# Kernel tuning notes

Hardware: AMD Instinct MI355X
Metric: run time of the kernel (lower is better)

The kernel has to match this reference:

```python
import jax, jax.numpy as jnp
import numpy as np

NUM_USERS = 50000
NUM_ITEMS = 20000
N_NODES = NUM_USERS + NUM_ITEMS
D = 128
CONTENT_DIM = 512
BATCH = 8192
N_EDGES = 500000
NEG_SLOPE = 0.2  # GATConv leaky_relu slope


def setup_inputs() -> dict:
    key = jax.random.key(0)
    ks = jax.random.split(key, 16)
    return {
        "user_ids": jax.random.randint(ks[0], (BATCH,), 0, NUM_USERS),
        "item_ids": jax.random.randint(ks[1], (BATCH,), 0, NUM_ITEMS),
        "content_features": jax.random.normal(ks[2], (BATCH, CONTENT_DIM), jnp.float32),
        "edge_index": jax.random.randint(ks[3], (2, N_EDGES), 0, N_NODES),
        "user_emb_w": jax.random.normal(ks[4], (NUM_USERS, D), jnp.float32) * 0.05,
        "item_emb_w": jax.random.normal(ks[5], (NUM_ITEMS, D), jnp.float32) * 0.05,
        "content_proj_w": jax.random.normal(ks[6], (D, CONTENT_DIM), jnp.float32) * 0.04,
        "content_proj_b": jnp.zeros((D,), jnp.float32),
        "conv1_lin_w": jax.random.normal(ks[7], (2 * D, 2 * D), jnp.float32) * 0.06,
        "conv1_att_src": jax.random.normal(ks[8], (2, D), jnp.float32) * 0.1,
        "conv1_att_dst": jax.random.normal(ks[9], (2, D), jnp.float32) * 0.1,
        "conv1_bias": jnp.zeros((2 * D,), jnp.float32),
        "conv2_lin_w": jax.random.normal(ks[10], (D, 2 * D), jnp.float32) * 0.06,
        "conv2_att_src": jax.random.normal(ks[11], (1, D), jnp.float32) * 0.1,
        "conv2_att_dst": jax.random.normal(ks[12], (1, D), jnp.float32) * 0.1,
        "conv2_bias": jnp.zeros((D,), jnp.float32),
        "pred_w1": jax.random.normal(ks[13], (D, 3 * D), jnp.float32) * 0.05,
        "pred_b1": jnp.zeros((D,), jnp.float32),
        "pred_w2": jax.random.normal(ks[14], (1, D), jnp.float32) * 0.09,
        "pred_b2": jnp.zeros((1,), jnp.float32),
    }


def gat_conv(x, src, dst, lin_w, att_src, att_dst, bias, heads, out_ch):
    # PyG GATConv (shared lin for src/dst, concat=True, add_self_loops handled outside)
    n = x.shape[0]
    h = (x @ lin_w.T).reshape(n, heads, out_ch)          # [N,H,C]
    a_src = jnp.sum(h * att_src, axis=-1)                # [N,H]
    a_dst = jnp.sum(h * att_dst, axis=-1)                # [N,H]
    alpha = jax.nn.leaky_relu(a_src[src] + a_dst[dst], NEG_SLOPE)  # [E,H]
    # softmax over incoming edges of each destination node
    amax = jax.ops.segment_max(alpha, dst, num_segments=n)
    ex = jnp.exp(alpha - amax[dst])
    denom = jax.ops.segment_sum(ex, dst, num_segments=n)
    w = ex / denom[dst]                                  # [E,H]
    out = jax.ops.segment_sum(h[src] * w[:, :, None], dst, num_segments=n)
    return out.reshape(n, heads * out_ch) + bias


def _forward(user_ids, item_ids, edge_index, content_features, user_emb_w, item_emb_w,
             content_proj_w, content_proj_b, conv1_lin_w, conv1_att_src, conv1_att_dst,
             conv1_bias, conv2_lin_w, conv2_att_src, conv2_att_dst, conv2_bias,
             pred_w1, pred_b1, pred_w2, pred_b2):
    u_emb = user_emb_w[user_ids]                         # [B,D]
    i_emb = item_emb_w[item_ids]                         # [B,D]
    c_emb = content_features @ content_proj_w.T + content_proj_b  # [B,D]
    # scatter-init sparse node features (only batch nodes are nonzero, as in source)
    x = jnp.zeros((N_NODES, 2 * D), jnp.float32)
    x = x.at[user_ids].set(jnp.concatenate([u_emb, jnp.zeros_like(c_emb)], axis=1))
    x = x.at[NUM_USERS + item_ids].set(jnp.concatenate([i_emb, c_emb], axis=1))
    # add self loops (fill_value irrelevant: edge_weight unused by GATConv)
    loops = jnp.arange(N_NODES, dtype=edge_index.dtype)
    src = jnp.concatenate([edge_index[0], loops])
    dst = jnp.concatenate([edge_index[1], loops])
    x = jax.nn.elu(gat_conv(x, src, dst, conv1_lin_w, conv1_att_src, conv1_att_dst, conv1_bias, 2, D))
    # dropout inactive (eval mode)
    x = gat_conv(x, src, dst, conv2_lin_w, conv2_att_src, conv2_att_dst, conv2_bias, 1, D)
    combined = jnp.concatenate([u_emb, x[NUM_USERS + item_ids], x[user_ids]], axis=1)  # [B,3D]
    h = jax.nn.relu(combined @ pred_w1.T + pred_b1)
    return (h @ pred_w2.T + pred_b2).squeeze(-1)         # [B]


def reference(user_ids, item_ids, content_features, edge_index, user_emb_w, item_emb_w,
              content_proj_w, content_proj_b, conv1_lin_w, conv1_att_src, conv1_att_dst,
              conv1_bias, conv2_lin_w, conv2_att_src, conv2_att_dst, conv2_bias,
              pred_w1, pred_b1, pred_w2, pred_b2):
    return _forward(user_ids, item_ids, edge_index, content_features, user_emb_w, item_emb_w,
                    content_proj_w, content_proj_b, conv1_lin_w, conv1_att_src, conv1_att_dst,
                    conv1_bias, conv2_lin_w, conv2_att_src, conv2_att_dst, conv2_bias,
                    pred_w1, pred_b1, pred_w2, pred_b2)
```

## Files before the change

### kernel.cpp

```cpp
#include <hip/hip_runtime.h>
#include <hip/hip_bf16.h>

#define NU 50000
#define NI 20000
#define NN 70000
#define DD 128
#define BB 8192
#define EE 500000
#define ET 570000
#define NTASK 16384

__device__ __forceinline__ float lrelu(float x) { return x > 0.f ? x : 0.2f * x; }

typedef __attribute__((ext_vector_type(8))) short bf16x8;
typedef __attribute__((ext_vector_type(8))) unsigned short u16x8;
typedef __attribute__((ext_vector_type(4))) float f32x4;

__device__ __forceinline__ unsigned short f2bf_rne(float f) {
  unsigned int u = __builtin_bit_cast(unsigned int, f);
  u += 0x7FFFu + ((u >> 16) & 1u);
  return (unsigned short)(u >> 16);
}
__device__ __forceinline__ float bf2f(unsigned short h) {
  unsigned int u = ((unsigned int)h) << 16;
  return __builtin_bit_cast(float, u);
}

template <int GATHER, int MODE>
__global__ __launch_bounds__(256) void gemm_mfma(
    const float* __restrict__ A,
    const unsigned short* __restrict__ Bh, const unsigned short* __restrict__ Bl,
    const float* __restrict__ bias, float* __restrict__ C,
    unsigned short* __restrict__ Cb, int ldc,
    int M, int N, int K, int act,
    const int* __restrict__ idx0, const int* __restrict__ idx1,
    const int* __restrict__ mapv,
    const float* __restrict__ gA0, const float* __restrict__ gA1,
    const float* __restrict__ att_s, const float* __restrict__ att_d,
    float* __restrict__ a1s, float* __restrict__ a1d) {
  __shared__ __align__(16) unsigned short sAh[8][64][8];
  __shared__ __align__(16) unsigned short sAl[8][64][8];
  __shared__ __align__(16) unsigned short sBh[8][64][8];
  __shared__ __align__(16) unsigned short sBl[8][64][8];
  int tid = threadIdx.x;
  int bm = blockIdx.x * 64, bn = blockIdx.y * 64;
  int lane = tid & 63, w = tid >> 6;
  int wr = (w >> 1) * 32, wc = (w & 1) * 32;
  int fr = lane & 15, fk = lane >> 4;
  f32x4 acc[2][2] = {};

  for (int k0 = 0; k0 < K; k0 += 64) {
    __syncthreads();
#pragma unroll
    for (int t = 0; t < 2; t++) {
      int f = tid + t * 256;
      int row = f >> 3, kb = f & 7;
      int kg = k0 + kb * 8;
      const float* ap;
      if (GATHER == 1) {
        int sec = kg >> 7;
        int kc = kg & 127;
        int r = bm + row;
        if (sec == 0)      ap = &gA0[(size_t)idx0[r] * 128 + kc];
        else if (sec == 1) ap = &gA1[(size_t)mapv[NU + idx1[r]] * 128 + kc];
        else               ap = &gA1[(size_t)mapv[idx0[r]] * 128 + kc];
      } else if (GATHER == 2) {
        ap = &gA0[(size_t)idx0[bm + row] * K + kg];
      } else {
        ap = &A[(size_t)(bm + row) * K + kg];
      }
      float4 v0 = *reinterpret_cast<const float4*>(ap);
      float4 v1 = *reinterpret_cast<const float4*>(ap + 4);
      float vv[8] = {v0.x, v0.y, v0.z, v0.w, v1.x, v1.y, v1.z, v1.w};
      u16x8 hv, lv;
#pragma unroll
      for (int j = 0; j < 8; j++) {
        unsigned short hh = f2bf_rne(vv[j]);
        hv[j] = hh;
        lv[j] = (unsigned short)(__builtin_bit_cast(unsigned int, vv[j] - bf2f(hh)) >> 16);
      }
      *reinterpret_cast<u16x8*>(&sAh[kb][row][0]) = hv;
      *reinterpret_cast<u16x8*>(&sAl[kb][row][0]) = lv;
    }
#pragma unroll
    for (int t = 0; t < 2; t++) {
      int f = tid + t * 256;
      int row = f >> 3, kb = f & 7;
      int kg = k0 + kb * 8;
      *reinterpret_cast<u16x8*>(&sBh[kb][row][0]) =
          *reinterpret_cast<const u16x8*>(&Bh[(size_t)(bn + row) * K + kg]);
      *reinterpret_cast<u16x8*>(&sBl[kb][row][0]) =
          *reinterpret_cast<const u16x8*>(&Bl[(size_t)(bn + row) * K + kg]);
    }
    __syncthreads();
#pragma unroll
    for (int s = 0; s < 2; s++) {
      int kb = s * 4 + fk;
      bf16x8 ah0 = *reinterpret_cast<const bf16x8*>(&sAh[kb][wr + fr][0]);
// ... 29 lines not shown
      for (int i = 0; i < 2; i++) {
#pragma unroll
        for (int r = 0; r < 4; r++) {
          float v = acc[i][j][r];
          ps[i][r] += v * asc;
          pd[i][r] += v * adc;
          Cb[(size_t)(bm + wr + i * 16 + fk * 4 + r) * ldc + col] = f2bf_rne(v);
        }
      }
    }
#pragma unroll
    for (int o = 1; o < 16; o <<= 1) {
#pragma unroll
      for (int i = 0; i < 2; i++)
#pragma unroll
        for (int r = 0; r < 4; r++) {
          ps[i][r] += __shfl_xor(ps[i][r], o);
          pd[i][r] += __shfl_xor(pd[i][r], o);
        }
    }
    if (fr == 0) {
#pragma unroll
      for (int i = 0; i < 2; i++) {
#pragma unroll
        for (int r = 0; r < 4; r++) {
          int t = bm + wr + i * 16 + fk * 4 + r;
          int v = (t < BB) ? idx0[t] : NU + idx1[t - BB];
          if (mapv[v] == t) {
            atomicAdd(&a1s[(size_t)v * 2 + head], ps[i][r]);
            atomicAdd(&a1d[(size_t)v * 2 + head], pd[i][r]);
          }
        }
      }
    }
    return;
  }
#pragma unroll
  for (int j = 0; j < 2; j++) {
    int col = bn + wc + j * 16 + fr;
    float bj = bias ? bias[col] : 0.f;
#pragma unroll
    for (int i = 0; i < 2; i++) {
#pragma unroll
      for (int r = 0; r < 4; r++) {
        int row = bm + wr + i * 16 + fk * 4 + r;
        float v = acc[i][j][r] + bj;
        if (act == 1) v = fmaxf(v, 0.f);
        C[(size_t)row * ldc + col] = v;
      }
    }
  }
}

#define EB 2227
#define SPLB 832
#define XAB 4096
__global__ __launch_bounds__(256) void setup_kernel(
    const int* __restrict__ ei, const int* __restrict__ uid, const int* __restrict__ iid,
    int* __restrict__ deg, int* __restrict__ winner,
    const float* __restrict__ wc, unsigned short* wch, unsigned short* wcl,
    const float* __restrict__ w1, unsigned short* w1h, unsigned short* w1l,
    const float* __restrict__ w2, unsigned short* w2h, unsigned short* w2l,
    const float* __restrict__ pw1, unsigned short* p1h, unsigned short* p1l,
    const float* __restrict__ uemb, const float* __restrict__ iemb,
    float* __restrict__ Xa, int* __restrict__ map) {
  int bid = blockIdx.x, tid = threadIdx.x;
  if (bid < EB) {
    int e = bid * 256 + tid;
    if (e < BB) atomicMax(&winner[iid[e]], e);
    if (e >= ET) return;
    int dst = (e < EE) ? ei[EE + e] : (e - EE);
    atomicAdd(&deg[dst], 1);
    return;
  }
  if (bid < EB + SPLB) {
    int i = (bid - EB) * 256 + tid;
    const float* w; unsigned short* h; unsigned short* l; int idx;
    if (i < 65536) { w = wc; h = wch; l = wcl; idx = i; }
    else if (i < 131072) { w = w1; h = w1h; l = w1l; idx = i - 65536; }
    else if (i < 163840) { w = w2; h = w2h; l = w2l; idx = i - 131072; }
    else { w = pw1; h = p1h; l = p1l; idx = i - 163840; }
    float f = w[idx];
    unsigned short hh = f2bf_rne(f);
    h[idx] = hh;
    l[idx] = (unsigned short)(__builtin_bit_cast(unsigned int, f - bf2f(hh)) >> 16);
    return;
  }
  int t = (bid - EB - SPLB) * 4 + (tid >> 6);
  int lane = tid & 63;
  int c4 = lane * 4;
  if (t < BB) {
    int u = uid[t];
    float4 v = make_float4(0.f, 0.f, 0.f, 0.f);
    if (c4 < DD) v = *reinterpret_cast<const float4*>(&uemb[(size_t)u * DD + c4]);
    *reinterpret_cast<float4*>(&Xa[(size_t)t * 256 + c4]) = v;
    if (lane == 0) map[u] = t;
  } else {
    int it = iid[t - BB];
    if (c4 < DD) {
      float4 v = *reinterpret_cast<const float4*>(&iemb[(size_t)it * DD + c4]);
      *reinterpret_cast<float4*>(&Xa[(size_t)t * 256 + c4]) = v;
    }
    if (lane == 0) map[NU + it] = t;
  }
}

__global__ void rowstart_kernel(const int* __restrict__ deg, const int* __restrict__ winner,
                                const int* __restrict__ iid,
                                int* __restrict__ rowstart, int* __restrict__ fill,
                                int* __restrict__ counter, int* __restrict__ widx,
                                const float* __restrict__ w2,
                                const float* __restrict__ att2s, const float* __restrict__ att2d,
                                float* __restrict__ qs, float* __restrict__ qd) {
  int blk = blockIdx.x;
  if (blk == (NN + 255) / 256) {
    int k = threadIdx.x;
    float s = 0.f, d = 0.f;
#pragma unroll 4
    for (int j = 0; j < DD; j++) {
      float w = w2[(size_t)j * 256 + k];
      s += att2s[j] * w;
      d += att2d[j] * w;
    }
    qs[k] = s;
    qd[k] = d;
    return;
  }
  int v = blk * 256 + threadIdx.x;
  if (v < BB) widx[v] = winner[iid[v]];
  if (v >= NN) return;
  int s = atomicAdd(counter, deg[v]);
  rowstart[v] = s;
  fill[v] = s;
}

__global__ void fill_mark_kernel(const int* __restrict__ ei, int* __restrict__ fill,
                                 int* __restrict__ col, const int* __restrict__ map,
                                 unsigned char* __restrict__ needed) {
  int e = blockIdx.x * 256 + threadIdx.x;
  if (e >= ET) return;
  int src, dst;
  if (e < EE) { src = ei[e]; dst = ei[EE + e]; }
  else { src = e - EE; dst = src; }
  int pos = atomicAdd(&fill[dst], 1);
  col[pos] = src;
  if (map[dst] >= 0) needed[src] = 1;
}

__global__ __launch_bounds__(256) void conv1_agg_kernel(
    const int* __restrict__ col, const int* __restrict__ rowstart,
    const int* __restrict__ deg, const unsigned short* __restrict__ Hb,
    const int* __restrict__ map, const unsigned char* __restrict__ needed,
    const float* __restrict__ a1s, const float* __restrict__ a1d,
    const float* __restrict__ bias,
    const float* __restrict__ qs, const float* __restrict__ qd,
    unsigned short* __restrict__ x1b, float* __restrict__ a2s, float* __restrict__ a2d) {
  int v = blockIdx.x * 4 + (threadIdx.x >> 6);
  int lane = threadIdx.x & 63;
  if (!needed[v]) return;
  int head = lane >> 5;
  int d = deg[v], s0 = rowstart[v];
  float2 adv = *reinterpret_cast<const float2*>(&a1d[(size_t)v * 2]);
  float4 acc = make_float4(0.f, 0.f, 0.f, 0.f);
  float den;
  if (d <= 64) {
    bool act = lane < d;
    int ci = act ? col[s0 + lane] : 0;
    float2 asv = make_float2(0.f, 0.f);
    int ri = -1;
    if (act) {
      asv = *reinterpret_cast<const float2*>(&a1s[(size_t)ci * 2]);
      ri = map[ci];
    }
    float al0 = act ? lrelu(asv.x + adv.x) : -1e30f;
    float al1 = act ? lrelu(asv.y + adv.y) : -1e30f;
    float m0 = al0, m1 = al1;
#pragma unroll
    for (int o = 1; o < 64; o <<= 1) {
      m0 = fmaxf(m0, __shfl_xor(m0, o));
      m1 = fmaxf(m1, __shfl_xor(m1, o));
    }
    float ex0 = act ? __expf(al0 - m0) : 0.f;
    float ex1 = act ? __expf(al1 - m1) : 0.f;
    float cs0 = ex0, cs1 = ex1;
#pragma unroll
    for (int o = 1; o < 64; o <<= 1) {
      cs0 += __shfl_xor(cs0, o);
      cs1 += __shfl_xor(cs1, o);
    }
    den = head ? cs1 : cs0;
    for (int i2 = 0; i2 < d; i2++) {
      int r = __shfl(ri, i2);
      if (r >= 0) {
        float e0 = __shfl(ex0, i2), e1 = __shfl(ex1, i2);
        float ex = head ? e1 : e0;
        ushort4 hv = *reinterpret_cast<const ushort4*>(&Hb[((size_t)r << 8) + (lane << 2)]);
        acc.x += ex * bf2f(hv.x); acc.y += ex * bf2f(hv.y);
        acc.z += ex * bf2f(hv.z); acc.w += ex * bf2f(hv.w);
      }
    }
  } else {
    float m0 = -1e30f, m1 = -1e30f, den0 = 0.f, den1 = 0.f;
    for (int c0 = 0; c0 < d; c0 += 64) {
      int i = c0 + lane;
      bool act = i < d;
      int ci = act ? col[s0 + i] : 0;
      float2 asv = make_float2(0.f, 0.f);
      int ri = -1;
      if (act) {
        asv = *reinterpret_cast<const float2*>(&a1s[(size_t)ci * 2]);
        ri = map[ci];
      }
      float al0 = act ? lrelu(asv.x + adv.x) : -1e30f;
      float al1 = act ? lrelu(asv.y + adv.y) : -1e30f;
      float cm0 = al0, cm1 = al1;
#pragma unroll
      for (int o = 1; o < 64; o <<= 1) {
        cm0 = fmaxf(cm0, __shfl_xor(cm0, o));
        cm1 = fmaxf(cm1, __shfl_xor(cm1, o));
      }
      float nm0 = fmaxf(m0, cm0), nm1 = fmaxf(m1, cm1);
      float ex0 = act ? __expf(al0 - nm0) : 0.f;
      float ex1 = act ? __expf(al1 - nm1) : 0.f;
      float s0f = __expf(m0 - nm0), s1f = __expf(m1 - nm1);
      float cs0 = ex0, cs1 = ex1;
#pragma unroll
      for (int o = 1; o < 64; o <<= 1) {
        cs0 += __shfl_xor(cs0, o);
        cs1 += __shfl_xor(cs1, o);
      }
      den0 = den0 * s0f + cs0;
      den1 = den1 * s1f + cs1;
      float sc = head ? s1f : s0f;
      acc.x *= sc; acc.y *= sc; acc.z *= sc; acc.w *= sc;
      int n = min(64, d - c0);
      for (int i2 = 0; i2 < n; i2++) {
        int r = __shfl(ri, i2);
        if (r >= 0) {
          float e0 = __shfl(ex0, i2), e1 = __shfl(ex1, i2);
          float ex = head ? e1 : e0;
          ushort4 hv = *reinterpret_cast<const ushort4*>(&Hb[((size_t)r << 8) + (lane << 2)]);
          acc.x += ex * bf2f(hv.x); acc.y += ex * bf2f(hv.y);
          acc.z += ex * bf2f(hv.z); acc.w += ex * bf2f(hv.w);
        }
      }
      m0 = nm0; m1 = nm1;
    }
    den = head ? den1 : den0;
  }
  float inv = 1.f / den;
  float4 b4 = *reinterpret_cast<const float4*>(&bias[lane << 2]);
  float4 o;
  o.x = fmaf(acc.x, inv, b4.x);
  o.y = fmaf(acc.y, inv, b4.y);
  o.z = fmaf(acc.z, inv, b4.z);
  o.w = fmaf(acc.w, inv, b4.w);
  o.x = o.x > 0.f ? o.x : __expf(o.x) - 1.f;
  o.y = o.y > 0.f ? o.y : __expf(o.y) - 1.f;
  o.z = o.z > 0.f ? o.z : __expf(o.z) - 1.f;
  o.w = o.w > 0.f ? o.w : __expf(o.w) - 1.f;
  ushort4 st;
  st.x = f2bf_rne(o.x); st.y = f2bf_rne(o.y);
  st.z = f2bf_rne(o.z); st.w = f2bf_rne(o.w);
  *reinterpret_cast<ushort4*>(&x1b[((size_t)v << 8) + (lane << 2)]) = st;
  float4 sv = *reinterpret_cast<const float4*>(&qs[lane << 2]);
  float4 dv = *reinterpret_cast<const float4*>(&qd[lane << 2]);
  float ps = o.x * sv.x + o.y * sv.y + o.z * sv.z + o.w * sv.w;
  float pd = o.x * dv.x + o.y * dv.y + o.z * dv.z + o.w * dv.w;
#pragma unroll
  for (int of = 1; of < 64; of <<= 1) { ps += __shfl_xor(ps, of); pd += __shfl_xor(pd, of); }
  if (lane == 0) { a2s[v] = ps; a2d[v] = pd; }
}

__global__ __launch_bounds__(256) void conv2_agg_kernel(
    const int* __restrict__ uid, const int* __restrict__ iid,
    const int* __restrict__ col, const int* __restrict__ rowstart,
    const int* __restrict__ deg, const int* __restrict__ map,
    const unsigned short* __restrict__ x1b,
    const float* __restrict__ a2s, const float* __restrict__ a2d,
    float* __restrict__ agg) {
  int t = blockIdx.x * 4 + (threadIdx.x >> 6);
  int lane = threadIdx.x & 63;
  int v = (t < BB) ? uid[t] : NU + iid[t - BB];
  if (map[v] != t) return;
  int d = deg[v], s0 = rowstart[v];
  float ad = a2d[v];
  float4 acc = make_float4(0.f, 0.f, 0.f, 0.f);
  float den;
  if (d <= 64) {
    bool act = lane < d;
    int ci = act ? col[s0 + lane] : 0;
    float as = act ? a2s[ci] : 0.f;
    float al = act ? lrelu(as + ad) : -1e30f;
    float m = al;
#pragma unroll
    for (int o = 1; o < 64; o <<= 1) m = fmaxf(m, __shfl_xor(m, o));
    float ex = act ? __expf(al - m) : 0.f;
    float cs = ex;
#pragma unroll
    for (int o = 1; o < 64; o <<= 1) cs += __shfl_xor(cs, o);
    den = cs;
    for (int i2 = 0; i2 < d; i2++) {
      int r = __shfl(ci, i2);
      float e = __shfl(ex, i2);
      ushort4 hv = *reinterpret_cast<const ushort4*>(&x1b[((size_t)r << 8) + (lane << 2)]);
      acc.x += e * bf2f(hv.x); acc.y += e * bf2f(hv.y);
      acc.z += e * bf2f(hv.z); acc.w += e * bf2f(hv.w);
    }
  } else {
    float m = -1e30f; den = 0.f;
    for (int c0 = 0; c0 < d; c0 += 64) {
      int i = c0 + lane;
      bool act = i < d;
      int ci = act ? col[s0 + i] : 0;
      float as = act ? a2s[ci] : 0.f;
      float al = act ? lrelu(as + ad) : -1e30f;
      float cm = al;
#pragma unroll
      for (int o = 1; o < 64; o <<= 1) cm = fmaxf(cm, __shfl_xor(cm, o));
      float nm = fmaxf(m, cm);
      float ex = act ? __expf(al - nm) : 0.f;
      float sf = __expf(m - nm);
      float cs = ex;
#pragma unroll
      for (int o = 1; o < 64; o <<= 1) cs += __shfl_xor(cs, o);
      den = den * sf + cs;
      acc.x *= sf; acc.y *= sf; acc.z *= sf; acc.w *= sf;
      int n = min(64, d - c0);
      for (int i2 = 0; i2 < n; i2++) {
        int r = __shfl(ci, i2);
        float e = __shfl(ex, i2);
        ushort4 hv = *reinterpret_cast<const ushort4*>(&x1b[((size_t)r << 8) + (lane << 2)]);
        acc.x += e * bf2f(hv.x); acc.y += e * bf2f(hv.y);
        acc.z += e * bf2f(hv.z); acc.w += e * bf2f(hv.w);
      }
      m = nm;
    }
  }
  float inv = 1.f / den;
  float4 o = make_float4(acc.x * inv, acc.y * inv, acc.z * inv, acc.w * inv);
  *reinterpret_cast<float4*>(&agg[((size_t)t << 8) + (lane << 2)]) = o;
}

__global__ __launch_bounds__(256) void final_kernel(
    const float* __restrict__ ph, const float* __restrict__ w2,
    const float* __restrict__ b2, float* __restrict__ out) {
  int b = blockIdx.x * 4 + (threadIdx.x >> 6);
  int lane = threadIdx.x & 63;
  float2 hv = *reinterpret_cast<const float2*>(&ph[((size_t)b << 7) + (lane << 1)]);
  float2 wv = *reinterpret_cast<const float2*>(&w2[lane << 1]);
  float s = hv.x * wv.x + hv.y * wv.y;
  for (int o = 1; o < 64; o <<= 1) s += __shfl_xor(s, o);
  if (lane == 0) out[b] = s + b2[0];
}

extern "C" void kernel_launch(void* const* d_in, const int* in_sizes, int n_in,
                              void* d_out, int out_size, void* d_ws, size_t ws_size,
                              hipStream_t stream) {
  const int* uid = (const int*)d_in[0];
  const int* iid = (const int*)d_in[1];
  const float* content = (const float*)d_in[2];
  const int* ei = (const int*)d_in[3];
  const float* uemb = (const float*)d_in[4];
  const float* iemb = (const float*)d_in[5];
  const float* wc = (const float*)d_in[6];
  const float* bc = (const float*)d_in[7];
  const float* w1 = (const float*)d_in[8];
  const float* att1s = (const float*)d_in[9];
  const float* att1d = (const float*)d_in[10];
  const float* b1 = (const float*)d_in[11];
  const float* w2 = (const float*)d_in[12];
  const float* att2s = (const float*)d_in[13];
  const float* att2d = (const float*)d_in[14];
  const float* b2c = (const float*)d_in[15];
  const float* pw1 = (const float*)d_in[16];
  const float* pb1 = (const float*)d_in[17];
  const float* pw2 = (const float*)d_in[18];
  const float* pb2 = (const float*)d_in[19];
  float* out = (float*)d_out;
  char* ws = (char*)d_ws;

  size_t off = 0;
  auto alloc = [&](size_t bytes) {
    size_t o = off;
    off += (bytes + 255) & ~(size_t)255;
    return o;
  };
  size_t o_winner  = alloc(NI * 4);
  size_t o_map     = alloc(NN * 4);
  size_t o_a1s     = alloc((size_t)NN * 2 * 4);
  size_t o_a1d     = alloc((size_t)NN * 2 * 4);
  size_t o_deg     = alloc(NN * 4);
  size_t o_rs      = alloc(NN * 4);
  size_t o_fill    = alloc(NN * 4);
  size_t o_cnt     = alloc(4);
  size_t o_needed  = alloc(NN);
  size_t o_col     = alloc((size_t)ET * 4);
  size_t o_a2s     = alloc(NN * 4);
  size_t o_a2d     = alloc(NN * 4);
  size_t o_qs      = alloc(256 * 4);
  size_t o_qd      = alloc(256 * 4);
  size_t o_widx    = alloc(BB * 4);
  size_t o_wch = alloc(65536 * 2),  o_wcl = alloc(65536 * 2);
  size_t o_w1h = alloc(65536 * 2),  o_w1l = alloc(65536 * 2);
  size_t o_w2h = alloc(32768 * 2),  o_w2l = alloc(32768 * 2);
  size_t o_p1h = alloc(49152 * 2),  o_p1l = alloc(49152 * 2);
  size_t o_r1    = alloc(16777216 + 8388608);
  size_t o_xa    = o_r1;
  size_t o_hb    = o_r1 + 16777216;
  size_t o_agg   = o_r1;
  size_t o_out2c = o_r1 + 16777216;
  size_t o_ph    = o_r1;
  size_t o_x1b   = alloc((size_t)NN * 256 * 2);
  (void)ws_size; (void)in_sizes; (void)n_in; (void)out_size;

  int*   winner = (int*)(ws + o_winner);
  int*   map    = (int*)(ws + o_map);
  float* a1s    = (float*)(ws + o_a1s);
  float* a1d    = (float*)(ws + o_a1d);
  int*   deg    = (int*)(ws + o_deg);
  int*   rs     = (int*)(ws + o_rs);
  int*   fill   = (int*)(ws + o_fill);
  int*   cnt    = (int*)(ws + o_cnt);
  unsigned char* needed = (unsigned char*)(ws + o_needed);
  int*   col    = (int*)(ws + o_col);
  float* a2s    = (float*)(ws + o_a2s);
  float* a2d    = (float*)(ws + o_a2d);
  float* qs     = (float*)(ws + o_qs);
  float* qd     = (float*)(ws + o_qd);
  int*   widx   = (int*)(ws + o_widx);
  unsigned short* wch = (unsigned short*)(ws + o_wch);
  unsigned short* wcl = (unsigned short*)(ws + o_wcl);
  unsigned short* w1h = (unsigned short*)(ws + o_w1h);
  unsigned short* w1l = (unsigned short*)(ws + o_w1l);
  unsigned short* w2h = (unsigned short*)(ws + o_w2h);
  unsigned short* w2l = (unsigned short*)(ws + o_w2l);
  unsigned short* p1h = (unsigned short*)(ws + o_p1h);
  unsigned short* p1l = (unsigned short*)(ws + o_p1l);
  float* Xa     = (float*)(ws + o_xa);
  unsigned short* Hb = (unsigned short*)(ws + o_hb);
  float* agg    = (float*)(ws + o_agg);
  float* out2c  = (float*)(ws + o_out2c);
  float* ph     = (float*)(ws + o_ph);
  unsigned short* x1b = (unsigned short*)(ws + o_x1b);

  hipMemsetAsync(ws + o_winner, 0xFF, o_map - o_winner + (size_t)NN * 4, stream);
  hipMemsetAsync(ws + o_a1s, 0, o_a1d - o_a1s + (size_t)NN * 2 * 4, stream);
  hipMemsetAsync(ws + o_deg, 0, o_needed - o_deg + NN, stream);

  setup_kernel<<<EB + SPLB + XAB, 256, 0, stream>>>(
      ei, uid, iid, deg, winner,
      wc, wch, wcl, w1, w1h, w1l, w2, w2h, w2l, pw1, p1h, p1l,
      uemb, iemb, Xa, map);
  rowstart_kernel<<<(NN + 255) / 256 + 1, 256, 0, stream>>>(
      deg, winner, iid, rs, fill, cnt, widx, w2, att2s, att2d, qs, qd);
  {
    dim3 g(BB / 64, DD / 64);
    gemm_mfma<2, 0><<<g, 256, 0, stream>>>(
        nullptr, wch, wcl, bc, Xa + (size_t)BB * 256 + 128, nullptr, 256,
        BB, DD, 512, 0, widx, nullptr, nullptr, content, nullptr,
        nullptr, nullptr, nullptr, nullptr);
  }
  fill_mark_kernel<<<(ET + 255) / 256, 256, 0, stream>>>(ei, fill, col, map, needed);
  {
    dim3 g(NTASK / 64, 256 / 64);
    gemm_mfma<0, 1><<<g, 256, 0, stream>>>(
        Xa, w1h, w1l, nullptr, nullptr, Hb, 256,
        NTASK, 256, 256, 0, uid, iid, map, nullptr, nullptr,
        att1s, att1d, a1s, a1d);
  }
  conv1_agg_kernel<<<NN / 4, 256, 0, stream>>>(col, rs, deg, Hb, map, needed,
                                               a1s, a1d, b1, qs, qd, x1b, a2s, a2d);
  conv2_agg_kernel<<<NTASK / 4, 256, 0, stream>>>(uid, iid, col, rs, deg, map,
                                                  x1b, a2s, a2d, agg);
  {
    dim3 g(NTASK / 64, DD / 64);
    gemm_mfma<0, 0><<<g, 256, 0, stream>>>(
        agg, w2h, w2l, b2c, out2c, nullptr, 128,
        NTASK, DD, 256, 0, nullptr, nullptr, nullptr, nullptr, nullptr,
        nullptr, nullptr, nullptr, nullptr);
  }
  {
    dim3 g(BB / 64, DD / 64);
    gemm_mfma<1, 0><<<g, 256, 0, stream>>>(
        nullptr, p1h, p1l, pb1, ph, nullptr, 128,
        BB, DD, 384, 1, uid, iid, map, uemb, out2c,
        nullptr, nullptr, nullptr, nullptr);
  }
  final_kernel<<<BB / 4, 256, 0, stream>>>(ph, pw2, pb2, out);
}
```

Baseline: 220.5 us.

## Merge content GEMM with CSR fill and widen gather loads in aggregation

The content-projection GEMM and the CSR fill/mark pass are now one launch: the first blocks run the GEMM tile and the rest do the edge scatter, so the two independent stages can overlap and one launch is saved. In both GAT aggregation kernels, each half-wave now handles alternate neighbours with 16-byte bf16 loads (8 features per lane), and the two halves are combined with a cross-half shuffle at the end. This halves the serial neighbour loop length and widens the loads, at the cost of more registers and an extra reduction step.

```diff
diff --git a/kernel.cpp b/kernel.cpp
--- a/kernel.cpp
+++ b/kernel.cpp
@@ -27,7 +27,8 @@
 }
 
 template <int GATHER, int MODE>
-__global__ __launch_bounds__(256) void gemm_mfma(
+__device__ __forceinline__ void gemm_core(
+    int bm, int bn,
     const float* __restrict__ A,
     const unsigned short* __restrict__ Bh, const unsigned short* __restrict__ Bl,
     const float* __restrict__ bias, float* __restrict__ C,
@@ -43,7 +44,6 @@
   __shared__ __align__(16) unsigned short sBh[8][64][8];
   __shared__ __align__(16) unsigned short sBl[8][64][8];
   int tid = threadIdx.x;
-  int bm = blockIdx.x * 64, bn = blockIdx.y * 64;
   int lane = tid & 63, w = tid >> 6;
   int wr = (w >> 1) * 32, wc = (w & 1) * 32;
   int fr = lane & 15, fk = lane >> 4;
@@ -179,6 +179,48 @@
   }
 }
 
+template <int GATHER, int MODE>
+__global__ __launch_bounds__(256) void gemm_mfma(
+    const float* __restrict__ A,
+    const unsigned short* __restrict__ Bh, const unsigned short* __restrict__ Bl,
+    const float* __restrict__ bias, float* __restrict__ C,
+    unsigned short* __restrict__ Cb, int ldc,
+    int M, int N, int K, int act,
+    const int* __restrict__ idx0, const int* __restrict__ idx1,
+    const int* __restrict__ mapv,
+    const float* __restrict__ gA0, const float* __restrict__ gA1,
+    const float* __restrict__ att_s, const float* __restrict__ att_d,
+    float* __restrict__ a1s, float* __restrict__ a1d) {
+  gemm_core<GATHER, MODE>(blockIdx.x * 64, blockIdx.y * 64,
+                          A, Bh, Bl, bias, C, Cb, ldc, M, N, K, act,
+                          idx0, idx1, mapv, gA0, gA1, att_s, att_d, a1s, a1d);
+}
+
+#define GEMMB 256
+__global__ __launch_bounds__(256) void cembfill_kernel(
+    const unsigned short* __restrict__ wch, const unsigned short* __restrict__ wcl,
+    const float* __restrict__ bc, float* __restrict__ XaC,
+    const int* __restrict__ widx, const float* __restrict__ content,
+    const int* __restrict__ ei, int* __restrict__ fill, int* __restrict__ col,
+    const int* __restrict__ mapv, unsigned char* __restrict__ needed) {
+  int bid = blockIdx.x;
+  if (bid < GEMMB) {
+    gemm_core<2, 0>((bid >> 1) * 64, (bid & 1) * 64,
+                    nullptr, wch, wcl, bc, XaC, nullptr, 256,
+                    BB, DD, 512, 0, widx, nullptr, nullptr, content, nullptr,
+                    nullptr, nullptr, nullptr, nullptr);
+    return;
+  }
+  int e = (bid - GEMMB) * 256 + threadIdx.x;
+  if (e >= ET) return;
+  int src, dst;
+  if (e < EE) { src = ei[e]; dst = ei[EE + e]; }
+  else { src = e - EE; dst = src; }
+  int pos = atomicAdd(&fill[dst], 1);
+  col[pos] = src;
+  if (mapv[dst] >= 0) needed[src] = 1;
+}
+
 #define EB 2227
 #define SPLB 832
 #define XAB 4096
@@ -261,19 +303,6 @@
   fill[v] = s;
 }
 
-__global__ void fill_mark_kernel(const int* __restrict__ ei, int* __restrict__ fill,
-                                 int* __restrict__ col, const int* __restrict__ map,
-                                 unsigned char* __restrict__ needed) {
-  int e = blockIdx.x * 256 + threadIdx.x;
-  if (e >= ET) return;
-  int src, dst;
-  if (e < EE) { src = ei[e]; dst = ei[EE + e]; }
-  else { src = e - EE; dst = src; }
-  int pos = atomicAdd(&fill[dst], 1);
-  col[pos] = src;
-  if (map[dst] >= 0) needed[src] = 1;
-}
-
 __global__ __launch_bounds__(256) void conv1_agg_kernel(
     const int* __restrict__ col, const int* __restrict__ rowstart,
     const int* __restrict__ deg, const unsigned short* __restrict__ Hb,
@@ -285,10 +314,12 @@
   int v = blockIdx.x * 4 + (threadIdx.x >> 6);
   int lane = threadIdx.x & 63;
   if (!needed[v]) return;
-  int head = lane >> 5;
+  int half = lane >> 5;
+  int sub = lane & 31;
+  int chead = sub >> 4;
   int d = deg[v], s0 = rowstart[v];
   float2 adv = *reinterpret_cast<const float2*>(&a1d[(size_t)v * 2]);
-  float4 acc = make_float4(0.f, 0.f, 0.f, 0.f);
+  float acc[8] = {};
   float den;
   if (d <= 64) {
     bool act = lane < d;
@@ -315,15 +346,17 @@
       cs0 += __shfl_xor(cs0, o);
       cs1 += __shfl_xor(cs1, o);
     }
-    den = head ? cs1 : cs0;
-    for (int i2 = 0; i2 < d; i2++) {
-      int r = __shfl(ri, i2);
+    den = chead ? cs1 : cs0;
+    int nIt = (d + 1) >> 1;
+    for (int i2 = 0; i2 < nIt; i2++) {
+      int s = 2 * i2 + half;
+      int r = __shfl(ri, s);
+      float e0 = __shfl(ex0, s), e1 = __shfl(ex1, s);
+      float ex = chead ? e1 : e0;
       if (r >= 0) {
-        float e0 = __shfl(ex0, i2), e1 = __shfl(ex1, i2);
-        float ex = head ? e1 : e0;
-        ushort4 hv = *reinterpret_cast<const ushort4*>(&Hb[((size_t)r << 8) + (lane << 2)]);
-        acc.x += ex * bf2f(hv.x); acc.y += ex * bf2f(hv.y);
-        acc.z += ex * bf2f(hv.z); acc.w += ex * bf2f(hv.w);
+        u16x8 hv = *reinterpret_cast<const u16x8*>(&Hb[((size_t)r << 8) + (sub << 3)]);
+#pragma unroll
+        for (int k = 0; k < 8; k++) acc[k] += ex * bf2f(hv[k]);
       }
     }
   } else {
@@ -358,44 +391,50 @@
       }
       den0 = den0 * s0f + cs0;
       den1 = den1 * s1f + cs1;
-      float sc = head ? s1f : s0f;
-      acc.x *= sc; acc.y *= sc; acc.z *= sc; acc.w *= sc;
+      float sc = chead ? s1f : s0f;
+#pragma unroll
+      for (int k = 0; k < 8; k++) acc[k] *= sc;
       int n = min(64, d - c0);
-      for (int i2 = 0; i2 < n; i2++) {
-        int r = __shfl(ri, i2);
+      int nIt = (n + 1) >> 1;
+      for (int i2 = 0; i2 < nIt; i2++) {
+        int s = 2 * i2 + half;
+        int r = __shfl(ri, s);
+        float e0 = __shfl(ex0, s), e1 = __shfl(ex1, s);
+        float ex = chead ? e1 : e0;
         if (r >= 0) {
-          float e0 = __shfl(ex0, i2), e1 = __shfl(ex1, i2);
-          float ex = head ? e1 : e0;
-          ushort4 hv = *reinterpret_cast<const ushort4*>(&Hb[((size_t)r << 8) + (lane << 2)]);
-          acc.x += ex * bf2f(hv.x); acc.y += ex * bf2f(hv.y);
-          acc.z += ex * bf2f(hv.z); acc.w += ex * bf2f(hv.w);
+          u16x8 hv = *reinterpret_cast<const u16x8*>(&Hb[((size_t)r << 8) + (sub << 3)]);
+#pragma unroll
+          for (int k = 0; k < 8; k++) acc[k] += ex * bf2f(hv[k]);
         }
       }
       m0 = nm0; m1 = nm1;
     }
-    den = head ? den1 : den0;
-  }
+    den = chead ? den1 : den0;
+  }
+#pragma unroll
+  for (int k = 0; k < 8; k++) acc[k] += __shfl_xor(acc[k], 32);
   float inv = 1.f / den;
-  float4 b4 = *reinterpret_cast<const float4*>(&bias[lane << 2]);
-  float4 o;
-  o.x = fmaf(acc.x, inv, b4.x);
-  o.y = fmaf(acc.y, inv, b4.y);
-  o.z = fmaf(acc.z, inv, b4.z);
-  o.w = fmaf(acc.w, inv, b4.w);
-  o.x = o.x > 0.f ? o.x : __expf(o.x) - 1.f;
-  o.y = o.y > 0.f ? o.y : __expf(o.y) - 1.f;
-  o.z = o.z > 0.f ? o.z : __expf(o.z) - 1.f;
-  o.w = o.w > 0.f ? o.w : __expf(o.w) - 1.f;
+  float o[8];
+  float4 b4a = *reinterpret_cast<const float4*>(&bias[sub << 3]);
+  float4 b4b = *reinterpret_cast<const float4*>(&bias[(sub << 3) + 4]);
+  float bb[8] = {b4a.x, b4a.y, b4a.z, b4a.w, b4b.x, b4b.y, b4b.z, b4b.w};
+#pragma unroll
+  for (int k = 0; k < 8; k++) {
+    float t = fmaf(acc[k], inv, bb[k]);
+    o[k] = t > 0.f ? t : __expf(t) - 1.f;
+  }
   ushort4 st;
-  st.x = f2bf_rne(o.x); st.y = f2bf_rne(o.y);
-  st.z = f2bf_rne(o.z); st.w = f2bf_rne(o.w);
-  *reinterpret_cast<ushort4*>(&x1b[((size_t)v << 8) + (lane << 2)]) = st;
-  float4 sv = *reinterpret_cast<const float4*>(&qs[lane << 2]);
-  float4 dv = *reinterpret_cast<const float4*>(&qd[lane << 2]);
-  float ps = o.x * sv.x + o.y * sv.y + o.z * sv.z + o.w * sv.w;
-  float pd = o.x * dv.x + o.y * dv.y + o.z * dv.z + o.w * dv.w;
-#pragma unroll
-  for (int of = 1; of < 64; of <<= 1) { ps += __shfl_xor(ps, of); pd += __shfl_xor(pd, of); }
+  st.x = f2bf_rne(o[half * 4 + 0]); st.y = f2bf_rne(o[half * 4 + 1]);
+  st.z = f2bf_rne(o[half * 4 + 2]); st.w = f2bf_rne(o[half * 4 + 3]);
+  *reinterpret_cast<ushort4*>(&x1b[((size_t)v << 8) + (sub << 3) + half * 4]) = st;
+  float ps = 0.f, pd = 0.f;
+#pragma unroll
+  for (int k = 0; k < 8; k++) {
+    ps += o[k] * qs[(sub << 3) + k];
+    pd += o[k] * qd[(sub << 3) + k];
+  }
+#pragma unroll
+  for (int of = 1; of < 32; of <<= 1) { ps += __shfl_xor(ps, of); pd += __shfl_xor(pd, of); }
   if (lane == 0) { a2s[v] = ps; a2d[v] = pd; }
 }
 
@@ -410,9 +449,10 @@
   int lane = threadIdx.x & 63;
   int v = (t < BB) ? uid[t] : NU + iid[t - BB];
   if (map[v] != t) return;
+  int half = lane >> 5, sub = lane & 31;
   int d = deg[v], s0 = rowstart[v];
   float ad = a2d[v];
-  float4 acc = make_float4(0.f, 0.f, 0.f, 0.f);
+  float acc[8] = {};
   float den;
   if (d <= 64) {
     bool act = lane < d;
@@ -427,12 +467,14 @@
 #pragma unroll
     for (int o = 1; o < 64; o <<= 1) cs += __shfl_xor(cs, o);
     den = cs;
-    for (int i2 = 0; i2 < d; i2++) {
-      int r = __shfl(ci, i2);
-      float e = __shfl(ex, i2);
-      ushort4 hv = *reinterpret_cast<const ushort4*>(&x1b[((size_t)r << 8) + (lane << 2)]);
-      acc.x += e * bf2f(hv.x); acc.y += e * bf2f(hv.y);
-      acc.z += e * bf2f(hv.z); acc.w += e * bf2f(hv.w);
+    int nIt = (d + 1) >> 1;
+    for (int i2 = 0; i2 < nIt; i2++) {
+      int s = 2 * i2 + half;
+      int r = __shfl(ci, s);
+      float e = __shfl(ex, s);
+      u16x8 hv = *reinterpret_cast<const u16x8*>(&x1b[((size_t)r << 8) + (sub << 3)]);
+#pragma unroll
+      for (int k = 0; k < 8; k++) acc[k] += e * bf2f(hv[k]);
     }
   } else {
     float m = -1e30f; den = 0.f;
@@ -452,21 +494,28 @@
 #pragma unroll
       for (int o = 1; o < 64; o <<= 1) cs += __shfl_xor(cs, o);
       den = den * sf + cs;
-      acc.x *= sf; acc.y *= sf; acc.z *= sf; acc.w *= sf;
+#pragma unroll
+      for (int k = 0; k < 8; k++) acc[k] *= sf;
       int n = min(64, d - c0);
-      for (int i2 = 0; i2 < n; i2++) {
-        int r = __shfl(ci, i2);
-        float e = __shfl(ex, i2);
-        ushort4 hv = *reinterpret_cast<const ushort4*>(&x1b[((size_t)r << 8) + (lane << 2)]);
-        acc.x += e * bf2f(hv.x); acc.y += e * bf2f(hv.y);
-        acc.z += e * bf2f(hv.z); acc.w += e * bf2f(hv.w);
+      int nIt = (n + 1) >> 1;
+      for (int i2 = 0; i2 < nIt; i2++) {
+        int s = 2 * i2 + half;
+        int r = __shfl(ci, s);
+        float e = __shfl(ex, s);
+        u16x8 hv = *reinterpret_cast<const u16x8*>(&x1b[((size_t)r << 8) + (sub << 3)]);
+#pragma unroll
+        for (int k = 0; k < 8; k++) acc[k] += e * bf2f(hv[k]);
       }
       m = nm;
     }
   }
+#pragma unroll
+  for (int k = 0; k < 8; k++) acc[k] += __shfl_xor(acc[k], 32);
   float inv = 1.f / den;
-  float4 o = make_float4(acc.x * inv, acc.y * inv, acc.z * inv, acc.w * inv);
-  *reinterpret_cast<float4*>(&agg[((size_t)t << 8) + (lane << 2)]) = o;
+  float4 st;
+  st.x = acc[half * 4 + 0] * inv; st.y = acc[half * 4 + 1] * inv;
+  st.z = acc[half * 4 + 2] * inv; st.w = acc[half * 4 + 3] * inv;
+  *reinterpret_cast<float4*>(&agg[((size_t)t << 8) + (sub << 3) + half * 4]) = st;
 }
 
 __global__ __launch_bounds__(256) void final_kernel(
@@ -581,14 +630,9 @@
       uemb, iemb, Xa, map);
   rowstart_kernel<<<(NN + 255) / 256 + 1, 256, 0, stream>>>(
       deg, winner, iid, rs, fill, cnt, widx, w2, att2s, att2d, qs, qd);
-  {
-    dim3 g(BB / 64, DD / 64);
-    gemm_mfma<2, 0><<<g, 256, 0, stream>>>(
-        nullptr, wch, wcl, bc, Xa + (size_t)BB * 256 + 128, nullptr, 256,
-        BB, DD, 512, 0, widx, nullptr, nullptr, content, nullptr,
-        nullptr, nullptr, nullptr, nullptr);
-  }
-  fill_mark_kernel<<<(ET + 255) / 256, 256, 0, stream>>>(ei, fill, col, map, needed);
+  cembfill_kernel<<<GEMMB + EB, 256, 0, stream>>>(
+      wch, wcl, bc, Xa + (size_t)BB * 256 + 128, widx, content,
+      ei, fill, col, map, needed);
   {
     dim3 g(NTASK / 64, 256 / 64);
     gemm_mfma<0, 1><<<g, 256, 0, stream>>>(
```

After: 212.5 us. 1.04x faster.

## Precompute GAT softmax edge weights in separate passes; merge content GEMM with edge fill

Applied to the files above, without the earlier changes.

Moves the per-destination attention softmax (max, exp, normalize) for both GAT layers out of the aggregation kernels into dedicated 8-lanes-per-node weight kernels that write normalized per-edge weights and remapped row indices. The aggregation kernels then become simple weighted gathers with no wavefront reductions or shuffles. The content-projection GEMM and the CSR fill/mark kernel are merged into a single launch via block-index dispatch so both can run concurrently. This adds two extra launches and extra global traffic for the per-edge weight buffers, and wbuf2 aliases rbuf memory.

```diff
diff --git a/kernel.cpp b/kernel.cpp
--- a/kernel.cpp
+++ b/kernel.cpp
@@ -27,7 +27,8 @@
 }
 
 template <int GATHER, int MODE>
-__global__ __launch_bounds__(256) void gemm_mfma(
+__device__ __forceinline__ void gemm_core(
+    int bm, int bn,
     const float* __restrict__ A,
     const unsigned short* __restrict__ Bh, const unsigned short* __restrict__ Bl,
     const float* __restrict__ bias, float* __restrict__ C,
@@ -43,7 +44,6 @@
   __shared__ __align__(16) unsigned short sBh[8][64][8];
   __shared__ __align__(16) unsigned short sBl[8][64][8];
   int tid = threadIdx.x;
-  int bm = blockIdx.x * 64, bn = blockIdx.y * 64;
   int lane = tid & 63, w = tid >> 6;
   int wr = (w >> 1) * 32, wc = (w & 1) * 32;
   int fr = lane & 15, fk = lane >> 4;
@@ -179,6 +179,48 @@
   }
 }
 
+template <int GATHER, int MODE>
+__global__ __launch_bounds__(256) void gemm_mfma(
+    const float* __restrict__ A,
+    const unsigned short* __restrict__ Bh, const unsigned short* __restrict__ Bl,
+    const float* __restrict__ bias, float* __restrict__ C,
+    unsigned short* __restrict__ Cb, int ldc,
+    int M, int N, int K, int act,
+    const int* __restrict__ idx0, const int* __restrict__ idx1,
+    const int* __restrict__ mapv,
+    const float* __restrict__ gA0, const float* __restrict__ gA1,
+    const float* __restrict__ att_s, const float* __restrict__ att_d,
+    float* __restrict__ a1s, float* __restrict__ a1d) {
+  gemm_core<GATHER, MODE>(blockIdx.x * 64, blockIdx.y * 64,
+                          A, Bh, Bl, bias, C, Cb, ldc, M, N, K, act,
+                          idx0, idx1, mapv, gA0, gA1, att_s, att_d, a1s, a1d);
+}
+
+#define GEMMB 256
+__global__ __launch_bounds__(256) void cembfill_kernel(
+    const unsigned short* __restrict__ wch, const unsigned short* __restrict__ wcl,
+    const float* __restrict__ bc, float* __restrict__ XaC,
+    const int* __restrict__ widx, const float* __restrict__ content,
+    const int* __restrict__ ei, int* __restrict__ fill, int* __restrict__ col,
+    const int* __restrict__ mapv, unsigned char* __restrict__ needed) {
+  int bid = blockIdx.x;
+  if (bid < GEMMB) {
+    gemm_core<2, 0>((bid >> 1) * 64, (bid & 1) * 64,
+                    nullptr, wch, wcl, bc, XaC, nullptr, 256,
+                    BB, DD, 512, 0, widx, nullptr, nullptr, content, nullptr,
+                    nullptr, nullptr, nullptr, nullptr);
+    return;
+  }
+  int e = (bid - GEMMB) * 256 + threadIdx.x;
+  if (e >= ET) return;
+  int src, dst;
+  if (e < EE) { src = ei[e]; dst = ei[EE + e]; }
+  else { src = e - EE; dst = src; }
+  int pos = atomicAdd(&fill[dst], 1);
+  col[pos] = src;
+  if (mapv[dst] >= 0) needed[src] = 1;
+}
+
 #define EB 2227
 #define SPLB 832
 #define XAB 4096
@@ -261,127 +303,127 @@
   fill[v] = s;
 }
 
-__global__ void fill_mark_kernel(const int* __restrict__ ei, int* __restrict__ fill,
-                                 int* __restrict__ col, const int* __restrict__ map,
-                                 unsigned char* __restrict__ needed) {
-  int e = blockIdx.x * 256 + threadIdx.x;
-  if (e >= ET) return;
-  int src, dst;
-  if (e < EE) { src = ei[e]; dst = ei[EE + e]; }
-  else { src = e - EE; dst = src; }
-  int pos = atomicAdd(&fill[dst], 1);
-  col[pos] = src;
-  if (map[dst] >= 0) needed[src] = 1;
+__global__ __launch_bounds__(256) void w1_kernel(
+    const int* __restrict__ col, const int* __restrict__ rowstart,
+    const int* __restrict__ deg, const int* __restrict__ map,
+    const unsigned char* __restrict__ needed,
+    const float* __restrict__ a1s, const float* __restrict__ a1d,
+    int* __restrict__ rbuf, float2* __restrict__ wbuf) {
+  int v = blockIdx.x * 32 + (threadIdx.x >> 3);
+  if (v >= NN || !needed[v]) return;
+  int gl = threadIdx.x & 7;
+  int d = deg[v], s0 = rowstart[v];
+  float2 adv = *reinterpret_cast<const float2*>(&a1d[(size_t)v * 2]);
+  float m0 = -1e30f, m1 = -1e30f;
+  for (int c0 = 0; c0 < d; c0 += 8) {
+    int i = c0 + gl;
+    if (i < d) {
+      float2 as = *reinterpret_cast<const float2*>(&a1s[(size_t)col[s0 + i] * 2]);
+      m0 = fmaxf(m0, lrelu(as.x + adv.x));
+      m1 = fmaxf(m1, lrelu(as.y + adv.y));
+    }
+  }
+#pragma unroll
+  for (int o = 1; o < 8; o <<= 1) {
+    m0 = fmaxf(m0, __shfl_xor(m0, o));
+    m1 = fmaxf(m1, __shfl_xor(m1, o));
+  }
+  float den0 = 0.f, den1 = 0.f;
+  for (int c0 = 0; c0 < d; c0 += 8) {
+    int i = c0 + gl;
+    if (i < d) {
+      int c = col[s0 + i];
+      float2 as = *reinterpret_cast<const float2*>(&a1s[(size_t)c * 2]);
+      float e0 = __expf(lrelu(as.x + adv.x) - m0);
+      float e1 = __expf(lrelu(as.y + adv.y) - m1);
+      den0 += e0; den1 += e1;
+      int r = map[c];
+      float msk = r >= 0 ? 1.f : 0.f;
+      rbuf[s0 + i] = r >= 0 ? r : 0;
+      wbuf[s0 + i] = make_float2(e0 * msk, e1 * msk);
+    }
+  }
+#pragma unroll
+  for (int o = 1; o < 8; o <<= 1) {
+    den0 += __shfl_xor(den0, o);
+    den1 += __shfl_xor(den1, o);
+  }
+  float i0 = 1.f / den0, i1 = 1.f / den1;
+  for (int c0 = 0; c0 < d; c0 += 8) {
+    int i = c0 + gl;
+    if (i < d) {
+      float2 w = wbuf[s0 + i];
+      wbuf[s0 + i] = make_float2(w.x * i0, w.y * i1);
+    }
+  }
+}
+
+__global__ __launch_bounds__(256) void w2_kernel(
+    const int* __restrict__ uid, const int* __restrict__ iid,
+    const int* __restrict__ col, const int* __restrict__ rowstart,
+    const int* __restrict__ deg, const int* __restrict__ map,
+    const float* __restrict__ a2s, const float* __restrict__ a2d,
+    float* __restrict__ wbuf2) {
+  int t = blockIdx.x * 32 + (threadIdx.x >> 3);
+  int v = (t < BB) ? uid[t] : NU + iid[t - BB];
+  if (map[v] != t) return;
+  int gl = threadIdx.x & 7;
+  int d = deg[v], s0 = rowstart[v];
+  float ad = a2d[v];
+  float m = -1e30f;
+  for (int c0 = 0; c0 < d; c0 += 8) {
+    int i = c0 + gl;
+    if (i < d) m = fmaxf(m, lrelu(a2s[col[s0 + i]] + ad));
+  }
+#pragma unroll
+  for (int o = 1; o < 8; o <<= 1) m = fmaxf(m, __shfl_xor(m, o));
+  float den = 0.f;
+  for (int c0 = 0; c0 < d; c0 += 8) {
+    int i = c0 + gl;
+    if (i < d) {
+      float e = __expf(lrelu(a2s[col[s0 + i]] + ad) - m);
+      den += e;
+      wbuf2[s0 + i] = e;
+    }
+  }
+#pragma unroll
+  for (int o = 1; o < 8; o <<= 1) den += __shfl_xor(den, o);
+  float inv = 1.f / den;
+  for (int c0 = 0; c0 < d; c0 += 8) {
+    int i = c0 + gl;
+    if (i < d) wbuf2[s0 + i] *= inv;
+  }
 }
 
 __global__ __launch_bounds__(256) void conv1_agg_kernel(
-    const int* __restrict__ col, const int* __restrict__ rowstart,
-    const int* __restrict__ deg, const unsigned short* __restrict__ Hb,
-    const int* __restrict__ map, const unsigned char* __restrict__ needed,
-    const float* __restrict__ a1s, const float* __restrict__ a1d,
+    const int* __restrict__ rowstart, const int* __restrict__ deg,
+    const unsigned short* __restrict__ Hb,
+    const unsigned char* __restrict__ needed,
+    const int* __restrict__ rbuf, const float2* __restrict__ wbuf,
     const float* __restrict__ bias,
     const float* __restrict__ qs, const float* __restrict__ qd,
     unsigned short* __restrict__ x1b, float* __restrict__ a2s, float* __restrict__ a2d) {
   int v = blockIdx.x * 4 + (threadIdx.x >> 6);
   int lane = threadIdx.x & 63;
   if (!needed[v]) return;
-  int head = lane >> 5;
+  int chead = lane >> 5;
   int d = deg[v], s0 = rowstart[v];
-  float2 adv = *reinterpret_cast<const float2*>(&a1d[(size_t)v * 2]);
   float4 acc = make_float4(0.f, 0.f, 0.f, 0.f);
-  float den;
-  if (d <= 64) {
-    bool act = lane < d;
-    int ci = act ? col[s0 + lane] : 0;
-    float2 asv = make_float2(0.f, 0.f);
-    int ri = -1;
-    if (act) {
-      asv = *reinterpret_cast<const float2*>(&a1s[(size_t)ci * 2]);
-      ri = map[ci];
-    }
-    float al0 = act ? lrelu(asv.x + adv.x) : -1e30f;
-    float al1 = act ? lrelu(asv.y + adv.y) : -1e30f;
-    float m0 = al0, m1 = al1;
-#pragma unroll
-    for (int o = 1; o < 64; o <<= 1) {
-      m0 = fmaxf(m0, __shfl_xor(m0, o));
-      m1 = fmaxf(m1, __shfl_xor(m1, o));
-    }
-    float ex0 = act ? __expf(al0 - m0) : 0.f;
-    float ex1 = act ? __expf(al1 - m1) : 0.f;
-    float cs0 = ex0, cs1 = ex1;
-#pragma unroll
-    for (int o = 1; o < 64; o <<= 1) {
-      cs0 += __shfl_xor(cs0, o);
-      cs1 += __shfl_xor(cs1, o);
-    }
-    den = head ? cs1 : cs0;
-    for (int i2 = 0; i2 < d; i2++) {
-      int r = __shfl(ri, i2);
-      if (r >= 0) {
-        float e0 = __shfl(ex0, i2), e1 = __shfl(ex1, i2);
-        float ex = head ? e1 : e0;
-        ushort4 hv = *reinterpret_cast<const ushort4*>(&Hb[((size_t)r << 8) + (lane << 2)]);
-        acc.x += ex * bf2f(hv.x); acc.y += ex * bf2f(hv.y);
-        acc.z += ex * bf2f(hv.z); acc.w += ex * bf2f(hv.w);
-      }
-    }
-  } else {
-    float m0 = -1e30f, m1 = -1e30f, den0 = 0.f, den1 = 0.f;
-    for (int c0 = 0; c0 < d; c0 += 64) {
-      int i = c0 + lane;
-      bool act = i < d;
-      int ci = act ? col[s0 + i] : 0;
-      float2 asv = make_float2(0.f, 0.f);
-      int ri = -1;
-      if (act) {
-        asv = *reinterpret_cast<const float2*>(&a1s[(size_t)ci * 2]);
-        ri = map[ci];
-      }
-      float al0 = act ? lrelu(asv.x + adv.x) : -1e30f;
-      float al1 = act ? lrelu(asv.y + adv.y) : -1e30f;
-      float cm0 = al0, cm1 = al1;
-#pragma unroll
-      for (int o = 1; o < 64; o <<= 1) {
-        cm0 = fmaxf(cm0, __shfl_xor(cm0, o));
-        cm1 = fmaxf(cm1, __shfl_xor(cm1, o));
-      }
-      float nm0 = fmaxf(m0, cm0), nm1 = fmaxf(m1, cm1);
-      float ex0 = act ? __expf(al0 - nm0) : 0.f;
-      float ex1 = act ? __expf(al1 - nm1) : 0.f;
-      float s0f = __expf(m0 - nm0), s1f = __expf(m1 - nm1);
-      float cs0 = ex0, cs1 = ex1;
-#pragma unroll
-      for (int o = 1; o < 64; o <<= 1) {
-        cs0 += __shfl_xor(cs0, o);
-        cs1 += __shfl_xor(cs1, o);
-      }
-      den0 = den0 * s0f + cs0;
-      den1 = den1 * s1f + cs1;
-      float sc = head ? s1f : s0f;
-      acc.x *= sc; acc.y *= sc; acc.z *= sc; acc.w *= sc;
-      int n = min(64, d - c0);
-      for (int i2 = 0; i2 < n; i2++) {
-        int r = __shfl(ri, i2);
-        if (r >= 0) {
-          float e0 = __shfl(ex0, i2), e1 = __shfl(ex1, i2);
-          float ex = head ? e1 : e0;
-          ushort4 hv = *reinterpret_cast<const ushort4*>(&Hb[((size_t)r << 8) + (lane << 2)]);
-          acc.x += ex * bf2f(hv.x); acc.y += ex * bf2f(hv.y);
-          acc.z += ex * bf2f(hv.z); acc.w += ex * bf2f(hv.w);
-        }
-      }
-      m0 = nm0; m1 = nm1;
-    }
-    den = head ? den1 : den0;
-  }
-  float inv = 1.f / den;
+#pragma unroll 2
+  for (int i = 0; i < d; i++) {
+    int r = rbuf[s0 + i];
+    float2 wv = wbuf[s0 + i];
+    float w = chead ? wv.y : wv.x;
+    ushort4 hv = *reinterpret_cast<const ushort4*>(&Hb[((size_t)r << 8) + (lane << 2)]);
+    acc.x += w * bf2f(hv.x); acc.y += w * bf2f(hv.y);
+    acc.z += w * bf2f(hv.z); acc.w += w * bf2f(hv.w);
+  }
   float4 b4 = *reinterpret_cast<const float4*>(&bias[lane << 2]);
   float4 o;
-  o.x = fmaf(acc.x, inv, b4.x);
-  o.y = fmaf(acc.y, inv, b4.y);
-  o.z = fmaf(acc.z, inv, b4.z);
-  o.w = fmaf(acc.w, inv, b4.w);
+  o.x = acc.x + b4.x;
+  o.y = acc.y + b4.y;
+  o.z = acc.z + b4.z;
+  o.w = acc.w + b4.w;
   o.x = o.x > 0.f ? o.x : __expf(o.x) - 1.f;
   o.y = o.y > 0.f ? o.y : __expf(o.y) - 1.f;
   o.z = o.z > 0.f ? o.z : __expf(o.z) - 1.f;
@@ -403,70 +445,23 @@
     const int* __restrict__ uid, const int* __restrict__ iid,
     const int* __restrict__ col, const int* __restrict__ rowstart,
     const int* __restrict__ deg, const int* __restrict__ map,
-    const unsigned short* __restrict__ x1b,
-    const float* __restrict__ a2s, const float* __restrict__ a2d,
+    const unsigned short* __restrict__ x1b, const float* __restrict__ wbuf2,
     float* __restrict__ agg) {
   int t = blockIdx.x * 4 + (threadIdx.x >> 6);
   int lane = threadIdx.x & 63;
   int v = (t < BB) ? uid[t] : NU + iid[t - BB];
   if (map[v] != t) return;
   int d = deg[v], s0 = rowstart[v];
-  float ad = a2d[v];
   float4 acc = make_float4(0.f, 0.f, 0.f, 0.f);
-  float den;
-  if (d <= 64) {
-    bool act = lane < d;
-    int ci = act ? col[s0 + lane] : 0;
-    float as = act ? a2s[ci] : 0.f;
-    float al = act ? lrelu(as + ad) : -1e30f;
-    float m = al;
-#pragma unroll
-    for (int o = 1; o < 64; o <<= 1) m = fmaxf(m, __shfl_xor(m, o));
-    float ex = act ? __expf(al - m) : 0.f;
-    float cs = ex;
-#pragma unroll
-    for (int o = 1; o < 64; o <<= 1) cs += __shfl_xor(cs, o);
-    den = cs;
-    for (int i2 = 0; i2 < d; i2++) {
-      int r = __shfl(ci, i2);
-      float e = __shfl(ex, i2);
-      ushort4 hv = *reinterpret_cast<const ushort4*>(&x1b[((size_t)r << 8) + (lane << 2)]);
-      acc.x += e * bf2f(hv.x); acc.y += e * bf2f(hv.y);
-      acc.z += e * bf2f(hv.z); acc.w += e * bf2f(hv.w);
-    }
-  } else {
-    float m = -1e30f; den = 0.f;
-    for (int c0 = 0; c0 < d; c0 += 64) {
-      int i = c0 + lane;
-      bool act = i < d;
-      int ci = act ? col[s0 + i] : 0;
-      float as = act ? a2s[ci] : 0.f;
-      float al = act ? lrelu(as + ad) : -1e30f;
-      float cm = al;
-#pragma unroll
-      for (int o = 1; o < 64; o <<= 1) cm = fmaxf(cm, __shfl_xor(cm, o));
-      float nm = fmaxf(m, cm);
-      float ex = act ? __expf(al - nm) : 0.f;
-      float sf = __expf(m - nm);
-      float cs = ex;
-#pragma unroll
-      for (int o = 1; o < 64; o <<= 1) cs += __shfl_xor(cs, o);
-      den = den * sf + cs;
-      acc.x *= sf; acc.y *= sf; acc.z *= sf; acc.w *= sf;
-      int n = min(64, d - c0);
-      for (int i2 = 0; i2 < n; i2++) {
-        int r = __shfl(ci, i2);
-        float e = __shfl(ex, i2);
-        ushort4 hv = *reinterpret_cast<const ushort4*>(&x1b[((size_t)r << 8) + (lane << 2)]);
-        acc.x += e * bf2f(hv.x); acc.y += e * bf2f(hv.y);
-        acc.z += e * bf2f(hv.z); acc.w += e * bf2f(hv.w);
-      }
-      m = nm;
-    }
-  }
-  float inv = 1.f / den;
-  float4 o = make_float4(acc.x * inv, acc.y * inv, acc.z * inv, acc.w * inv);
-  *reinterpret_cast<float4*>(&agg[((size_t)t << 8) + (lane << 2)]) = o;
+#pragma unroll 2
+  for (int i = 0; i < d; i++) {
+    int c = col[s0 + i];
+    float w = wbuf2[s0 + i];
+    ushort4 hv = *reinterpret_cast<const ushort4*>(&x1b[((size_t)c << 8) + (lane << 2)]);
+    acc.x += w * bf2f(hv.x); acc.y += w * bf2f(hv.y);
+    acc.z += w * bf2f(hv.z); acc.w += w * bf2f(hv.w);
+  }
+  *reinterpret_cast<float4*>(&agg[((size_t)t << 8) + (lane << 2)]) = acc;
 }
 
 __global__ __launch_bounds__(256) void final_kernel(
@@ -523,6 +518,8 @@
   size_t o_cnt     = alloc(4);
   size_t o_needed  = alloc(NN);
   size_t o_col     = alloc((size_t)ET * 4);
+  size_t o_rbuf    = alloc((size_t)ET * 4);
+  size_t o_wbuf    = alloc((size_t)ET * 8);
   size_t o_a2s     = alloc(NN * 4);
   size_t o_a2d     = alloc(NN * 4);
   size_t o_qs      = alloc(256 * 4);
@@ -551,6 +548,9 @@
   int*   cnt    = (int*)(ws + o_cnt);
   unsigned char* needed = (unsigned char*)(ws + o_needed);
   int*   col    = (int*)(ws + o_col);
+  int*   rbuf   = (int*)(ws + o_rbuf);
+  float* wbuf2  = (float*)(ws + o_rbuf);
+  float2* wbuf  = (float2*)(ws + o_wbuf);
   float* a2s    = (float*)(ws + o_a2s);
   float* a2d    = (float*)(ws + o_a2d);
   float* qs     = (float*)(ws + o_qs);
@@ -581,14 +581,9 @@
       uemb, iemb, Xa, map);
   rowstart_kernel<<<(NN + 255) / 256 + 1, 256, 0, stream>>>(
       deg, winner, iid, rs, fill, cnt, widx, w2, att2s, att2d, qs, qd);
-  {
-    dim3 g(BB / 64, DD / 64);
-    gemm_mfma<2, 0><<<g, 256, 0, stream>>>(
-        nullptr, wch, wcl, bc, Xa + (size_t)BB * 256 + 128, nullptr, 256,
-        BB, DD, 512, 0, widx, nullptr, nullptr, content, nullptr,
-        nullptr, nullptr, nullptr, nullptr);
-  }
-  fill_mark_kernel<<<(ET + 255) / 256, 256, 0, stream>>>(ei, fill, col, map, needed);
+  cembfill_kernel<<<GEMMB + EB, 256, 0, stream>>>(
+      wch, wcl, bc, Xa + (size_t)BB * 256 + 128, widx, content,
+      ei, fill, col, map, needed);
   {
     dim3 g(NTASK / 64, 256 / 64);
     gemm_mfma<0, 1><<<g, 256, 0, stream>>>(
@@ -596,10 +591,14 @@
         NTASK, 256, 256, 0, uid, iid, map, nullptr, nullptr,
         att1s, att1d, a1s, a1d);
   }
-  conv1_agg_kernel<<<NN / 4, 256, 0, stream>>>(col, rs, deg, Hb, map, needed,
-                                               a1s, a1d, b1, qs, qd, x1b, a2s, a2d);
+  w1_kernel<<<(NN + 31) / 32, 256, 0, stream>>>(col, rs, deg, map, needed,
+                                                a1s, a1d, rbuf, wbuf);
+  conv1_agg_kernel<<<NN / 4, 256, 0, stream>>>(rs, deg, Hb, needed, rbuf, wbuf,
+                                               b1, qs, qd, x1b, a2s, a2d);
+  w2_kernel<<<NTASK / 32, 256, 0, stream>>>(uid, iid, col, rs, deg, map,
+                                            a2s, a2d, wbuf2);
   conv2_agg_kernel<<<NTASK / 4, 256, 0, stream>>>(uid, iid, col, rs, deg, map,
-                                                  x1b, a2s, a2d, agg);
+                                                  x1b, wbuf2, agg);
   {
     dim3 g(NTASK / 64, DD / 64);
     gemm_mfma<0, 0><<<g, 256, 0, stream>>>(
```

Result: slower. 238.4 us (+8.1%).
